# Kernel tuning notes

Hardware: AMD Instinct MI355X
Metric: run time of the kernel (lower is better)

## Reference

```python
import jax, jax.numpy as jnp
import numpy as np

N_NODES = 100000
N_EDGES = 1600000
IN_FEAT, HIDDEN, N_CLASSES = 512, 32, 16


def setup_inputs() -> dict:
    key = jax.random.key(0)
    k1, k2, k3, k4 = jax.random.split(key, 4)
    x = jax.random.normal(k1, (N_NODES, IN_FEAT), dtype=jnp.float32)
    edge_index = jax.random.randint(k2, (2, N_EDGES), 0, N_NODES, dtype=jnp.int64)
    W1 = jax.random.normal(k3, (IN_FEAT, HIDDEN), dtype=jnp.float32) * (1.0 / np.sqrt(IN_FEAT))
    b1 = jnp.zeros((HIDDEN,), dtype=jnp.float32)
    W2 = jax.random.normal(k4, (HIDDEN, N_CLASSES), dtype=jnp.float32) * (1.0 / np.sqrt(HIDDEN))
    b2 = jnp.zeros((N_CLASSES,), dtype=jnp.float32)
    return {"x": x, "edge_index": edge_index, "W1": W1, "b1": b1, "W2": W2, "b2": b2}


def gcn_conv(x, row, col, norm, W, b, n_nodes):
    # linear transform first (PyG GCNConv order), then gather-scale-scatter
    h = x @ W                                   # [N, F_out]
    msg = h[row] * norm[:, None]                # edge-gather + normalize
    out = jax.ops.segment_sum(msg, col, num_segments=n_nodes)
    return out + b


def gcn_norm(edge_index, n_nodes):
    # add self-loops, symmetric normalization deg^{-1/2}[row]*deg^{-1/2}[col]
    loop = jnp.arange(n_nodes, dtype=edge_index.dtype)
    row = jnp.concatenate([edge_index[0], loop])
    col = jnp.concatenate([edge_index[1], loop])
    deg = jax.ops.segment_sum(jnp.ones_like(col, dtype=jnp.float32), col, num_segments=n_nodes)
    dis = jnp.where(deg > 0, jax.lax.rsqrt(jnp.maximum(deg, 1.0)), 0.0)
    norm = dis[row] * dis[col]
    return row, col, norm


def reference(x, edge_index, W1, b1, W2, b2):
    n_nodes = x.shape[0]
    row, col, norm = gcn_norm(edge_index, n_nodes)
    h = gcn_conv(x, row, col, norm, W1, b1, n_nodes)
    h = jax.nn.relu(h)
    # dropout p=0.5 in eval mode -> identity (deterministic baseline)
    h = gcn_conv(h, row, col, norm, W2, b2, n_nodes)
    return jax.nn.log_softmax(h, axis=1)
```

## Files before the change

kernel.cpp:

```cpp
#include <hip/hip_runtime.h>
#include <hip/hip_bf16.h>

#define NN 100000
#define NE 1600000
#define FIN 512
#define FH 32
#define FC 16
#define NCB ((NE / 4 + 255) / 256)
#define M_SL 128
#define SLICE (NE / M_SL)
#define QSL (SLICE / 4)
#define PSZ 32768
#define NP ((NN + PSZ - 1) / PSZ)
#define NHB (M_SL * NP)
#define NGB1 ((NN + 63) / 64)
#define XW (NN / 4)
#define XSB ((XW + 255) / 256)
#define SOS_NB 98
#define SCALE_B ((NN * FH / 4 + 1023) / 1024)

typedef __attribute__((ext_vector_type(8))) short bf16x8;
typedef __attribute__((ext_vector_type(4))) float f32x4;

__device__ inline unsigned short f2bf(float f) {
    unsigned u = __float_as_uint(f);
    return (unsigned short)((u + 0x7FFFu + ((u >> 16) & 1u)) >> 16);
}
__device__ inline float bf2f(unsigned short u) {
    return __uint_as_float(((unsigned)u) << 16);
}
__device__ inline unsigned pk2bf(float a, float b) {
    __hip_bfloat162 p = __float22bfloat162_rn(make_float2(a, b));
    union { __hip_bfloat162 h; unsigned u; } c;
    c.h = p;
    return c.u;
}


__global__ __launch_bounds__(256) void k_prep(const float* __restrict__ W1,
                                              unsigned short* __restrict__ wbuf) {
    for (int idx = threadIdx.x; idx < 16 * 2 * 64; idx += 256) {
        int s = idx >> 7;
        int t = (idx >> 6) & 1;
        int l = idx & 63;
        int k0 = s * 32 + (l >> 4) * 8;
        int c = t * 16 + (l & 15);
        bf16x8 w;
#pragma unroll
        for (int i = 0; i < 8; ++i) w[i] = (short)f2bf(W1[(size_t)(k0 + i) * FH + c]);
        *(bf16x8*)(wbuf + (size_t)idx * 8) = w;
    }
}


__global__ __launch_bounds__(256) void k_hist_gemm1(const int* __restrict__ col,
                                                    unsigned char* __restrict__ ghist,
                                                    unsigned char* __restrict__ rank,
                                                    const float* __restrict__ x,
                                                    const unsigned short* __restrict__ wbuf,
                                                    float* __restrict__ h1) {
    __shared__ int sh[PSZ / 4];

    if (blockIdx.x >= NGB1) {
        int hb = blockIdx.x - NGB1;
        int p = hb / M_SL;
        int m = hb % M_SL;
        int base = p * PSZ;
        int nb = min(PSZ, NN - base);
        int nw = (nb + 3) >> 2;
        unsigned* shw = (unsigned*)sh;
        for (int i = threadIdx.x; i < nw; i += 256) shw[i] = 0u;
        __syncthreads();
        const int4* c4p = (const int4*)(col + m * SLICE);
        for (int it = 0; it < (QSL + 255) / 256; ++it) {
            int q = it * 256 + threadIdx.x;
            if (q < QSL) {
                int4 c4 = c4p[q];
                int e = m * SLICE + q * 4;
                int cc[4] = {c4.x, c4.y, c4.z, c4.w};
#pragma unroll
                for (int u = 0; u < 4; ++u) {
                    int d = cc[u] - base;
                    if ((unsigned)d < (unsigned)nb) {
                        int sft = 8 * (d & 3);
                        unsigned old = atomicAdd(&shw[d >> 2], 1u << sft);
                        rank[e + u] = (unsigned char)((old >> sft) & 0xFFu);
                    }
                }
            }
        }
        __syncthreads();
        unsigned* gdst = (unsigned*)(ghist + (size_t)m * NN + base);
        for (int i = threadIdx.x; i < nw; i += 256) gdst[i] = shw[i];
        return;
    }

    unsigned short* lb = (unsigned short*)sh;
    for (int i = threadIdx.x; i < 2048; i += 256)
        ((int4*)lb)[i] = ((const int4*)wbuf)[i];
    __syncthreads();

    int wave = threadIdx.x >> 6;
    int lane = threadIdx.x & 63;
    int rowbase = blockIdx.x * 64 + wave * 16;
    int arow = rowbase + (lane & 15);
    int arowc = min(arow, NN - 1);
    int kgrp = (lane >> 4) * 8;

    f32x4 acc0 = {0.f, 0.f, 0.f, 0.f};
    f32x4 acc1 = {0.f, 0.f, 0.f, 0.f};
    const float* xrow = x + (size_t)arowc * FIN + kgrp;

    for (int sg = 0; sg < 16; sg += 4) {
        float4 av[8];
#pragma unroll
        for (int u = 0; u < 4; ++u) {
            av[2 * u]     = *(const float4*)(xrow + (sg + u) * 32);
            av[2 * u + 1] = *(const float4*)(xrow + (sg + u) * 32 + 4);
        }
#pragma unroll
        for (int u = 0; u < 4; ++u) {
            const float* s0 = (const float*)&av[2 * u];
            const float* s1 = (const float*)&av[2 * u + 1];
            union { bf16x8 v; unsigned w[4]; } af;
            af.w[0] = pk2bf(s0[0], s0[1]);
            af.w[1] = pk2bf(s0[2], s0[3]);
            af.w[2] = pk2bf(s1[0], s1[1]);
            af.w[3] = pk2bf(s1[2], s1[3]);
            int s = sg + u;
            bf16x8 b0 = *(const bf16x8*)(lb + ((size_t)(s * 2 + 0) * 64 + lane) * 8);
            bf16x8 b1 = *(const bf16x8*)(lb + ((size_t)(s * 2 + 1) * 64 + lane) * 8);
            acc0 = __builtin_amdgcn_mfma_f32_16x16x32_bf16(af.v, b0, acc0, 0, 0, 0);
            acc1 = __builtin_amdgcn_mfma_f32_16x16x32_bf16(af.v, b1, acc1, 0, 0, 0);
        }
    }

    int crow = rowbase + (lane >> 4) * 4;
    int ccol = lane & 15;
#pragma unroll
    for (int r = 0; r < 4; ++r) {
        if (crow + r < NN) {
            h1[(size_t)(crow + r) * FH + ccol] = acc0[r];
            h1[(size_t)(crow + r) * FH + 16 + ccol] = acc1[r];
        }
    }
}


__global__ __launch_bounds__(256) void k_xscan(unsigned* __restrict__ ghistw,
                                               int* __restrict__ cnt,
                                               float* __restrict__ dis,
                                               int* __restrict__ part) {
    __shared__ int red[256];
    int widx = blockIdx.x * 256 + threadIdx.x;
    int tot = 0;
    if (widx < XW) {
        unsigned s0 = 0, s1 = 0, s2 = 0, s3 = 0;
        unsigned* p = ghistw + widx;
        for (int m = 0; m < M_SL; ++m) {
            unsigned w = p[(size_t)m * XW];
            p[(size_t)m * XW] = s0 | (s1 << 8) | (s2 << 16) | (s3 << 24);
            s0 += w & 0xFFu; s1 += (w >> 8) & 0xFFu;
            s2 += (w >> 16) & 0xFFu; s3 += (w >> 24) & 0xFFu;
        }
        int c0 = widx * 4;
        *(int4*)(cnt + c0) = make_int4(s0, s1, s2, s3);
        *(float4*)(dis + c0) = make_float4(rsqrtf((float)s0 + 1.f), rsqrtf((float)s1 + 1.f),
                                           rsqrtf((float)s2 + 1.f), rsqrtf((float)s3 + 1.f));
        tot = s0 + s1 + s2 + s3;
    }
    red[threadIdx.x] = tot;
    __syncthreads();
    for (int st = 128; st > 0; st >>= 1) {
        if (threadIdx.x < st) red[threadIdx.x] += red[threadIdx.x + st];
        __syncthreads();
    }
    if (threadIdx.x == 0) part[blockIdx.x] = red[0];
}


__global__ __launch_bounds__(1024) void k_scan_off_scale(const int* __restrict__ cnt,
                                                         const int* __restrict__ part,
                                                         int* __restrict__ off,
                                                         const float4* __restrict__ h1,
                                                         ushort4* __restrict__ h1s,
                                                         const float* __restrict__ dis) {
    int bid = blockIdx.x;
    if (bid < SOS_NB) {
        __shared__ int s[1024];
        __shared__ int sp[128];
        if (threadIdx.x < 128) sp[threadIdx.x] = (threadIdx.x < XSB) ? part[threadIdx.x] : 0;
        __syncthreads();
        for (int st = 1; st < 128; st <<= 1) {
            int a = (threadIdx.x < 128 && threadIdx.x >= st) ? sp[threadIdx.x - st] : 0;
            __syncthreads();
            if (threadIdx.x < 128) sp[threadIdx.x] += a;
            __syncthreads();
        }
        int pbase = (bid == 0) ? 0 : sp[bid - 1];
        int i = bid * 1024 + threadIdx.x;
        int v = (i < NN) ? cnt[i] : 0;
        s[threadIdx.x] = v;
        __syncthreads();
        for (int st = 1; st < 1024; st <<= 1) {
            int a = (threadIdx.x >= st) ? s[threadIdx.x - st] : 0;
            __syncthreads();
            s[threadIdx.x] += a;
            __syncthreads();
        }
        if (i < NN) off[i] = pbase + s[threadIdx.x] - v;
        if (i == NN - 1) off[NN] = pbase + s[threadIdx.x];
    } else {
        int idx = (bid - SOS_NB) * 1024 + threadIdx.x;
        if (idx < NN * FH / 4) {
            float4 v = h1[idx];
            float d = dis[idx >> 3];
            union { ushort4 s4; unsigned u[2]; } o;
            o.u[0] = pk2bf(v.x * d, v.y * d);
            o.u[1] = pk2bf(v.z * d, v.w * d);
            h1s[idx] = o.s4;
        }
    }
}


__global__ void k_fill(const int* __restrict__ row, const int* __restrict__ col,
                       const unsigned char* __restrict__ rank,
                       const int* __restrict__ off,
                       const unsigned char* __restrict__ ghist,
                       int* __restrict__ esrc) {
    int i = blockIdx.x * blockDim.x + threadIdx.x;
    if (i >= NE / 4) return;
    int m = i / QSL;
    int4 r4 = ((const int4*)row)[i];
    int4 c4 = ((const int4*)col)[i];
    uchar4 rk4 = ((const uchar4*)rank)[i];
    int rr[4] = {r4.x, r4.y, r4.z, r4.w};
    int cc[4] = {c4.x, c4.y, c4.z, c4.w};
    int rk[4] = {rk4.x, rk4.y, rk4.z, rk4.w};
    int o4[4], bp[4];
#pragma unroll
    for (int u = 0; u < 4; ++u) o4[u] = off[cc[u]];
#pragma unroll
    for (int u = 0; u < 4; ++u) bp[u] = ghist[(size_t)m * NN + cc[u]];
#pragma unroll
    for (int u = 0; u < 4; ++u) esrc[o4[u] + bp[u] + rk[u]] = rr[u];
}


__global__ __launch_bounds__(256) void k_gather1g2(const int* __restrict__ off,
                                                   const int* __restrict__ esrc,
                                                   const unsigned* __restrict__ h1s2,
                                                   const float* __restrict__ dis,
                                                   const float* __restrict__ b1,
                                                   const float* __restrict__ W2,
                                                   float* __restrict__ h2s) {
    __shared__ float w2l[FH * FC];
    __shared__ float hrl[16][FH + 2];
    for (int i = threadIdx.x; i < FH * FC; i += 256) w2l[i] = W2[i];

    int ng = threadIdx.x >> 4;
    int l = threadIdx.x & 15;
    int g = blockIdx.x * 16 + ng;
    int s0 = off[g], s1 = off[g + 1];
    const unsigned* hp = h1s2 + l;
    float ax0 = 0.f, ay0 = 0.f, ax1 = 0.f, ay1 = 0.f;
    float ax2 = 0.f, ay2 = 0.f, ax3 = 0.f, ay3 = 0.f;
    int i = s0;
    for (; i + 3 < s1; i += 4) {
        int r0 = esrc[i], r1 = esrc[i + 1], r2 = esrc[i + 2], r3 = esrc[i + 3];
        unsigned w0 = hp[(size_t)r0 * 16];
        unsigned w1 = hp[(size_t)r1 * 16];
        unsigned w2 = hp[(size_t)r2 * 16];
        unsigned w3 = hp[(size_t)r3 * 16];
        ax0 += bf2f((unsigned short)w0); ay0 += bf2f((unsigned short)(w0 >> 16));
        ax1 += bf2f((unsigned short)w1); ay1 += bf2f((unsigned short)(w1 >> 16));
        ax2 += bf2f((unsigned short)w2); ay2 += bf2f((unsigned short)(w2 >> 16));
        ax3 += bf2f((unsigned short)w3); ay3 += bf2f((unsigned short)(w3 >> 16));
    }
    for (; i < s1; ++i) {
        unsigned w = hp[(size_t)esrc[i] * 16];
        ax0 += bf2f((unsigned short)w); ay0 += bf2f((unsigned short)(w >> 16));
    }
    unsigned ws = hp[(size_t)g * 16];
    float accx = ax0 + ax1 + ax2 + ax3 + bf2f((unsigned short)ws);
    float accy = ay0 + ay1 + ay2 + ay3 + bf2f((unsigned short)(ws >> 16));
    float dg = dis[g];
    float2 bb = ((const float2*)b1)[l];
    float vx = dg * accx + bb.x;
    float vy = dg * accy + bb.y;
    float2 vr = make_float2(vx > 0.f ? vx : 0.f, vy > 0.f ? vy : 0.f);
    *(float2*)&hrl[ng][2 * l] = vr;
    __syncthreads();

    int n2 = threadIdx.x >> 4;
    int j = threadIdx.x & 15;
    int g2 = blockIdx.x * 16 + n2;
    float s = 0.0f;
#pragma unroll
    for (int k = 0; k < FH; ++k) s += hrl[n2][k] * w2l[k * FC + j];
    h2s[(size_t)g2 * FC + j] = s * dis[g2];
}


__global__ __launch_bounds__(256) void k_gather2(const int* __restrict__ off,
                                                 const int* __restrict__ esrc,
                                                 const float* __restrict__ h2s,
                                                 const float* __restrict__ dis,
                                                 const float* __restrict__ b2,
                                                 float* __restrict__ out) {
    int ng = threadIdx.x >> 3;
    int l = threadIdx.x & 7;
    int g = blockIdx.x * 32 + ng;
    int s0 = off[g], s1 = off[g + 1];
    const float2* hp = (const float2*)h2s + l;
    float ax0 = 0.f, ay0 = 0.f, ax1 = 0.f, ay1 = 0.f;
    float ax2 = 0.f, ay2 = 0.f, ax3 = 0.f, ay3 = 0.f;
    int i = s0;
    for (; i + 3 < s1; i += 4) {
        int r0 = esrc[i], r1 = esrc[i + 1], r2 = esrc[i + 2], r3 = esrc[i + 3];
        float2 t0 = hp[(size_t)r0 * 8];
        float2 t1 = hp[(size_t)r1 * 8];
        float2 t2 = hp[(size_t)r2 * 8];
        float2 t3 = hp[(size_t)r3 * 8];
        ax0 += t0.x; ay0 += t0.y;
        ax1 += t1.x; ay1 += t1.y;
        ax2 += t2.x; ay2 += t2.y;
        ax3 += t3.x; ay3 += t3.y;
    }
    for (; i < s1; ++i) {
        float2 t = hp[(size_t)esrc[i] * 8];
        ax0 += t.x; ay0 += t.y;
    }
    float2 ts = hp[(size_t)g * 8];
    float accx = ax0 + ax1 + ax2 + ax3 + ts.x;
    float accy = ay0 + ay1 + ay2 + ay3 + ts.y;
    float dg = dis[g];
    float2 bb = ((const float2*)b2)[l];
    float vx = dg * accx + bb.x;
    float vy = dg * accy + bb.y;
    float m = fmaxf(vx, vy);
#pragma unroll
    for (int o = 1; o < 8; o <<= 1) m = fmaxf(m, __shfl_xor(m, o, 8));
    float e = __expf(vx - m) + __expf(vy - m);
    float s = e;
#pragma unroll
    for (int o = 1; o < 8; o <<= 1) s += __shfl_xor(s, o, 8);
    float ls = logf(s);
    ((float2*)out)[(size_t)g * 8 + l] = make_float2(vx - m - ls, vy - m - ls);
}

extern "C" void kernel_launch(void* const* d_in, const int* in_sizes, int n_in,
                              void* d_out, int out_size, void* d_ws, size_t ws_size,
                              hipStream_t stream) {
    const float* x  = (const float*)d_in[0];
    const int*   ei = (const int*)d_in[1];
    const float* W1 = (const float*)d_in[2];
    const float* b1 = (const float*)d_in[3];
    const float* W2 = (const float*)d_in[4];
    const float* b2 = (const float*)d_in[5];
    float* out = (float*)d_out;

    const int* row = ei;
    const int* col = ei + NE;

    int* base = (int*)d_ws;
    unsigned char* ghist = (unsigned char*)base;
    unsigned char* rank  = ghist + (size_t)M_SL * NN;
    int*   cnt   = base + 3200000 + 400000;
    int*   off   = cnt + NN;
    int*   part  = off + NN + 8;
    float* dis   = (float*)(part + 128);
    unsigned short* wbuf = (unsigned short*)(dis + NN);
    float* h1    = (float*)(wbuf + 16384);
    unsigned short* h1s = (unsigned short*)(h1 + (size_t)NN * FH);
    int*   esrc  = (int*)(h1s + (size_t)NN * FH);
    float* h2s   = h1;

    const int B = 256;

    k_prep<<<1, B, 0, stream>>>(W1, wbuf);
    k_hist_gemm1<<<NGB1 + NHB, B, 0, stream>>>(col, ghist, rank, x, wbuf, h1);
    k_xscan<<<XSB, B, 0, stream>>>((unsigned*)ghist, cnt, dis, part);
    k_scan_off_scale<<<SOS_NB + SCALE_B, 1024, 0, stream>>>(cnt, part, off,
                                                            (const float4*)h1, (ushort4*)h1s, dis);
    k_fill<<<NCB, B, 0, stream>>>(row, col, rank, off, ghist, esrc);
    k_gather1g2<<<NN / 16, B, 0, stream>>>(off, esrc, (const unsigned*)h1s, dis, b1, W2, h2s);
    k_gather2<<<NN / 32, B, 0, stream>>>(off, esrc, h2s, dis, b2, out);
}
```

Baseline: 186.2 us.

## Store GEMM1 output as packed bf16 and cut histogram slices to 32

The first GEMM now writes its output as packed bf16 pairs (column c with c+16) instead of fp32. This halves h1 write and read traffic in the scale pass, and the gather kernel's unpacking is adjusted to the new interleaved layout. The number of histogram edge slices drops from 128 to 32, which shrinks the per-slice byte histograms, the workspace, and the column-scan loop. The cost is an extra bf16 rounding before the degree scaling, plus longer serial work per histogram block with fewer blocks in flight.

```diff
diff --git a/kernel.cpp b/kernel.cpp
--- a/kernel.cpp
+++ b/kernel.cpp
@@ -7,7 +7,7 @@
 #define FH 32
 #define FC 16
 #define NCB ((NE / 4 + 255) / 256)
-#define M_SL 128
+#define M_SL 32
 #define SLICE (NE / M_SL)
 #define QSL (SLICE / 4)
 #define PSZ 32768
@@ -17,7 +17,7 @@
 #define XW (NN / 4)
 #define XSB ((XW + 255) / 256)
 #define SOS_NB 98
-#define SCALE_B ((NN * FH / 4 + 1023) / 1024)
+#define SCALE_B ((NN * 8 + 1023) / 1024)
 
 typedef __attribute__((ext_vector_type(8))) short bf16x8;
 typedef __attribute__((ext_vector_type(4))) float f32x4;
@@ -58,7 +58,7 @@
                                                     unsigned char* __restrict__ rank,
                                                     const float* __restrict__ x,
                                                     const unsigned short* __restrict__ wbuf,
-                                                    float* __restrict__ h1) {
+                                                    unsigned* __restrict__ h1p) {
     __shared__ int sh[PSZ / 4];
 
     if (blockIdx.x >= NGB1) {
@@ -139,10 +139,8 @@
     int ccol = lane & 15;
 #pragma unroll
     for (int r = 0; r < 4; ++r) {
-        if (crow + r < NN) {
-            h1[(size_t)(crow + r) * FH + ccol] = acc0[r];
-            h1[(size_t)(crow + r) * FH + 16 + ccol] = acc1[r];
-        }
+        if (crow + r < NN)
+            h1p[(size_t)(crow + r) * 16 + ccol] = pk2bf(acc0[r], acc1[r]);
     }
 }
 
@@ -157,6 +155,7 @@
     if (widx < XW) {
         unsigned s0 = 0, s1 = 0, s2 = 0, s3 = 0;
         unsigned* p = ghistw + widx;
+#pragma unroll 4
         for (int m = 0; m < M_SL; ++m) {
             unsigned w = p[(size_t)m * XW];
             p[(size_t)m * XW] = s0 | (s1 << 8) | (s2 << 16) | (s3 << 24);
@@ -182,8 +181,8 @@
 __global__ __launch_bounds__(1024) void k_scan_off_scale(const int* __restrict__ cnt,
                                                          const int* __restrict__ part,
                                                          int* __restrict__ off,
-                                                         const float4* __restrict__ h1,
-                                                         ushort4* __restrict__ h1s,
+                                                         const uint2* __restrict__ h1p2,
+                                                         uint2* __restrict__ h1s2,
                                                          const float* __restrict__ dis) {
     int bid = blockIdx.x;
     if (bid < SOS_NB) {
@@ -212,13 +211,15 @@
         if (i == NN - 1) off[NN] = pbase + s[threadIdx.x];
     } else {
         int idx = (bid - SOS_NB) * 1024 + threadIdx.x;
-        if (idx < NN * FH / 4) {
-            float4 v = h1[idx];
+        if (idx < NN * 8) {
+            uint2 v = h1p2[idx];
             float d = dis[idx >> 3];
-            union { ushort4 s4; unsigned u[2]; } o;
-            o.u[0] = pk2bf(v.x * d, v.y * d);
-            o.u[1] = pk2bf(v.z * d, v.w * d);
-            h1s[idx] = o.s4;
+            float a0 = bf2f((unsigned short)v.x), a1 = bf2f((unsigned short)(v.x >> 16));
+            float a2 = bf2f((unsigned short)v.y), a3 = bf2f((unsigned short)(v.y >> 16));
+            uint2 o;
+            o.x = pk2bf(a0 * d, a1 * d);
+            o.y = pk2bf(a2 * d, a3 * d);
+            h1s2[idx] = o;
         }
     }
 }
@@ -250,7 +251,7 @@
 
 __global__ __launch_bounds__(256) void k_gather1g2(const int* __restrict__ off,
                                                    const int* __restrict__ esrc,
-                                                   const unsigned* __restrict__ h1s2,
+                                                   const unsigned* __restrict__ h1s,
                                                    const float* __restrict__ dis,
                                                    const float* __restrict__ b1,
                                                    const float* __restrict__ W2,
@@ -263,7 +264,7 @@
     int l = threadIdx.x & 15;
     int g = blockIdx.x * 16 + ng;
     int s0 = off[g], s1 = off[g + 1];
-    const unsigned* hp = h1s2 + l;
+    const unsigned* hp = h1s + l;
     float ax0 = 0.f, ay0 = 0.f, ax1 = 0.f, ay1 = 0.f;
     float ax2 = 0.f, ay2 = 0.f, ax3 = 0.f, ay3 = 0.f;
     int i = s0;
@@ -286,11 +287,10 @@
     float accx = ax0 + ax1 + ax2 + ax3 + bf2f((unsigned short)ws);
     float accy = ay0 + ay1 + ay2 + ay3 + bf2f((unsigned short)(ws >> 16));
     float dg = dis[g];
-    float2 bb = ((const float2*)b1)[l];
-    float vx = dg * accx + bb.x;
-    float vy = dg * accy + bb.y;
-    float2 vr = make_float2(vx > 0.f ? vx : 0.f, vy > 0.f ? vy : 0.f);
-    *(float2*)&hrl[ng][2 * l] = vr;
+    float vx = dg * accx + b1[l];
+    float vy = dg * accy + b1[l + 16];
+    hrl[ng][l] = vx > 0.f ? vx : 0.f;
+    hrl[ng][l + 16] = vy > 0.f ? vy : 0.f;
     __syncthreads();
 
     int n2 = threadIdx.x >> 4;
@@ -367,24 +367,24 @@
     int* base = (int*)d_ws;
     unsigned char* ghist = (unsigned char*)base;
     unsigned char* rank  = ghist + (size_t)M_SL * NN;
-    int*   cnt   = base + 3200000 + 400000;
+    int*   cnt   = base + 800000 + 400000;
     int*   off   = cnt + NN;
     int*   part  = off + NN + 8;
     float* dis   = (float*)(part + 128);
     unsigned short* wbuf = (unsigned short*)(dis + NN);
-    float* h1    = (float*)(wbuf + 16384);
-    unsigned short* h1s = (unsigned short*)(h1 + (size_t)NN * FH);
-    int*   esrc  = (int*)(h1s + (size_t)NN * FH);
-    float* h2s   = h1;
+    unsigned* h1p = (unsigned*)(wbuf + 16384);
+    unsigned* h1s = h1p + (size_t)NN * 16;
+    int*   esrc  = (int*)(h1s + (size_t)NN * 16);
+    float* h2s   = (float*)h1p;
 
     const int B = 256;
 
     k_prep<<<1, B, 0, stream>>>(W1, wbuf);
-    k_hist_gemm1<<<NGB1 + NHB, B, 0, stream>>>(col, ghist, rank, x, wbuf, h1);
+    k_hist_gemm1<<<NGB1 + NHB, B, 0, stream>>>(col, ghist, rank, x, wbuf, h1p);
     k_xscan<<<XSB, B, 0, stream>>>((unsigned*)ghist, cnt, dis, part);
     k_scan_off_scale<<<SOS_NB + SCALE_B, 1024, 0, stream>>>(cnt, part, off,
-                                                            (const float4*)h1, (ushort4*)h1s, dis);
+                                                            (const uint2*)h1p, (uint2*)h1s, dis);
     k_fill<<<NCB, B, 0, stream>>>(row, col, rank, off, ghist, esrc);
-    k_gather1g2<<<NN / 16, B, 0, stream>>>(off, esrc, (const unsigned*)h1s, dis, b1, W2, h2s);
+    k_gather1g2<<<NN / 16, B, 0, stream>>>(off, esrc, h1s, dis, b1, W2, h2s);
     k_gather2<<<NN / 32, B, 0, stream>>>(off, esrc, h2s, dis, b2, out);
 }
```

Result: faster. 171.7 us (-7.8%).
